# Performance work log

Hardware: AMD Instinct MI355X
Metric: run time of the kernel (lower is better)

Reference implementation:

```python
import jax, jax.numpy as jnp
import numpy as np

B, N, NUM_CLASSES = 2, 131072, 2
SCORE_THR, IOU_THR, OUT_NUM = 0.05, 0.7, 2000
NEG = -1e9  # sentinel for suppressed / below-threshold scores


def _decode(deltas, anchors):
    h = anchors[..., 2] - anchors[..., 0]
    w = anchors[..., 3] - anchors[..., 1]
    cy = (anchors[..., 2] + anchors[..., 0]) * 0.5
    cx = (anchors[..., 3] + anchors[..., 1]) * 0.5
    d = deltas * jnp.array([0.1, 0.1, 0.2, 0.2], dtype=deltas.dtype)
    cy = cy + d[..., 0] * h
    cx = cx + d[..., 1] * w
    h = h * jnp.exp(d[..., 2])
    w = w * jnp.exp(d[..., 3])
    return jnp.stack([cy - h * 0.5, cx - w * 0.5, cy + h * 0.5, cx + w * 0.5], axis=-1)


def _iou(box, boxes):
    # box [4] vs boxes [N,4] -> [N]
    y1 = jnp.maximum(box[0], boxes[:, 0])
    x1 = jnp.maximum(box[1], boxes[:, 1])
    y2 = jnp.minimum(box[2], boxes[:, 2])
    x2 = jnp.minimum(box[3], boxes[:, 3])
    inter = jnp.maximum(y2 - y1, 0.0) * jnp.maximum(x2 - x1, 0.0)
    a1 = (box[2] - box[0]) * (box[3] - box[1])
    a2 = (boxes[:, 2] - boxes[:, 0]) * (boxes[:, 3] - boxes[:, 1])
    return inter / (a1 + a2 - inter + 1e-8)


def _nms_single(boxes, scores, logits):
    # greedy NMS (= tf.image.non_max_suppression), then gather + pad_to_fixed_size
    live0 = jnp.where(scores > SCORE_THR, scores, NEG)

    def step(live, _):
        best = jnp.argmax(live)
        ok = live[best] > NEG * 0.5
        iou = _iou(boxes[best], boxes)
        live = jnp.where((iou > IOU_THR) & ok, NEG, live)
        live = live.at[best].set(NEG)
        return live, (best.astype(jnp.int32), ok.astype(boxes.dtype))

    _, (sel, valid) = jax.lax.scan(step, live0, None, length=OUT_NUM)
    vb = valid[:, None]  # [OUT_NUM,1] pad tag: 1 for real rows, 0 for padding
    out_boxes = boxes[sel] * vb
    out_scores = scores[sel][:, None] * vb
    out_logits = logits[sel] * vb
    return (jnp.concatenate([out_boxes, vb], axis=-1),
            jnp.concatenate([out_scores, vb], axis=-1),
            jnp.concatenate([out_logits, vb], axis=-1))


def _forward(deltas, class_logits, anchors):
    probs = jax.nn.softmax(class_logits, axis=-1)
    fg_scores = jnp.max(probs[..., 1:], axis=-1)  # [B,N]
    boxes = _decode(deltas, anchors)              # [B,N,4]
    return jax.vmap(_nms_single)(boxes, fg_scores, class_logits)


def setup_inputs() -> dict:
    key = jax.random.key(0)
    k1, k2, k3, k4, k5, k6 = jax.random.split(key, 6)
    deltas = jax.random.normal(k1, (B, N, 4), jnp.float32) * 0.5
    class_logits = jax.random.normal(k2, (B, N, NUM_CLASSES), jnp.float32)
    cy = jax.random.uniform(k3, (B, N), minval=0.0, maxval=800.0)
    cx = jax.random.uniform(k4, (B, N), minval=0.0, maxval=800.0)
    h = jax.random.uniform(k5, (B, N), minval=16.0, maxval=256.0)
    w = jax.random.uniform(k6, (B, N), minval=16.0, maxval=256.0)
    anchors = jnp.stack([cy - h * 0.5, cx - w * 0.5, cy + h * 0.5, cx + w * 0.5], axis=-1)
    return {"deltas": deltas, "class_logits": class_logits, "anchors": anchors}


def reference(deltas, class_logits, anchors):
    return _forward(deltas, class_logits, anchors)
```

## Files before the change

### kernel.cpp

```cpp
#include <hip/hip_runtime.h>
#include <stdint.h>
#include <stddef.h>

#define BATCH 2
#define NELEM 131072
#define OUT_NUM 2000
#define KCAP 32
#define PREWIN 16384
#define KPRE_W (PREWIN / 64)

__device__ __forceinline__ float exp32cr(float x) { return (float)exp((double)x); }

__device__ __forceinline__ bool iou_gt(float by1, float bx1, float by2, float bx2,
                                       float cy1, float cx1, float cy2, float cx2) {
    float y1 = fmaxf(by1, cy1), x1 = fmaxf(bx1, cx1);
    float y2 = fminf(by2, cy2), x2 = fminf(bx2, cx2);
    float ih = __fsub_rn(y2, y1), iw = __fsub_rn(x2, x1);
    if (ih <= 0.0f || iw <= 0.0f) return false;
    float inter = __fmul_rn(ih, iw);
    float a1 = __fmul_rn(__fsub_rn(by2, by1), __fsub_rn(bx2, bx1));
    float a2 = __fmul_rn(__fsub_rn(cy2, cy1), __fsub_rn(cx2, cx1));
    float den = __fadd_rn(__fsub_rn(__fadd_rn(a1, a2), inter), 1e-8f);
    float rhs = __fmul_rn(0.7f, den);
    if (inter > __fmul_rn(rhs, 1.0001f)) return true;
    if (inter < __fmul_rn(rhs, 0.9999f)) return false;
    return __fdiv_rn(inter, den) > 0.7f;
}
__device__ __forceinline__ bool iou_gt4(float4 a, float4 c) {
    return iou_gt(a.x, a.y, a.z, a.w, c.x, c.y, c.z, c.w);
}

__device__ __forceinline__ bool maybe4(float4 A, float4 C) {
    float dy = fabsf((A.x + A.z) - (C.x + C.z));
    float dx = fabsf((A.y + A.w) - (C.y + C.w));
    float hs = (A.z - A.x) + (C.z - C.x);
    float ws = (A.w - A.y) + (C.w - C.y);
    return (dy < 0.19f * hs) && (dx < 0.19f * ws);
}

__device__ __forceinline__ void decode_f(const float* __restrict__ deltas,
                                         const float* __restrict__ anchors,
                                         size_t gi, float* bx) {
    float a0 = anchors[4 * gi], a1 = anchors[4 * gi + 1];
    float a2 = anchors[4 * gi + 2], a3 = anchors[4 * gi + 3];
    float h = __fsub_rn(a2, a0), w = __fsub_rn(a3, a1);
    float cy = __fmul_rn(__fadd_rn(a2, a0), 0.5f);
    float cx = __fmul_rn(__fadd_rn(a3, a1), 0.5f);
    float d0 = __fmul_rn(deltas[4 * gi], 0.1f);
    float d1 = __fmul_rn(deltas[4 * gi + 1], 0.1f);
    float d2 = __fmul_rn(deltas[4 * gi + 2], 0.2f);
    float d3 = __fmul_rn(deltas[4 * gi + 3], 0.2f);
    cy = __fadd_rn(cy, __fmul_rn(d0, h));
    cx = __fadd_rn(cx, __fmul_rn(d1, w));
    h = __fmul_rn(h, exp32cr(d2));
    w = __fmul_rn(w, exp32cr(d3));
    bx[0] = __fsub_rn(cy, __fmul_rn(h, 0.5f));
    bx[1] = __fsub_rn(cx, __fmul_rn(w, 0.5f));
    bx[2] = __fadd_rn(cy, __fmul_rn(h, 0.5f));
    bx[3] = __fadd_rn(cx, __fmul_rn(w, 0.5f));
}

__device__ __forceinline__ float score_f(const float* __restrict__ logits, size_t gi) {
    float l0 = logits[2 * gi], l1 = logits[2 * gi + 1];
    float m = fmaxf(l0, l1);
    float e0 = exp32cr(__fsub_rn(l0, m));
    float e1 = exp32cr(__fsub_rn(l1, m));
    return __fdiv_rn(e1, __fadd_rn(e0, e1));
}

__global__ __launch_bounds__(256) void prep_kernel(
    const float* __restrict__ logits, uint64_t* __restrict__ keys,
    uint32_t* __restrict__ flag, uint32_t* __restrict__ state) {
    int i = blockIdx.x * 256 + threadIdx.x;
    if (i == 0) *flag = 0;
    if (i < 32) state[i] = 0;
    if (i >= BATCH * NELEM) return;
    float s = score_f(logits, (size_t)i);
    uint32_t idx = (uint32_t)(i & (NELEM - 1));
    uint64_t key = 0;
    if (s > 0.05f)
        key = ((uint64_t)__float_as_uint(s) << 17) | ((~idx) & 0x1FFFFu);
    keys[i] = key;
}

__global__ __launch_bounds__(1024) void bitonic_local_sort4(uint64_t* __restrict__ keys) {
    __shared__ uint64_t sh[4096];
    const int t = threadIdx.x;
    const size_t base = (size_t)blockIdx.x * 4096;
    for (int e = t; e < 4096; e += 1024) sh[e] = keys[base + e];
    __syncthreads();
    const int gb = (int)(base & (NELEM - 1));
    for (int k = 2; k <= 4096; k <<= 1) {
        for (int j = k >> 1; j >= 1; j >>= 1) {
            for (int pp = t; pp < 2048; pp += 1024) {
                int a = ((pp & ~(j - 1)) << 1) | (pp & (j - 1));
                bool ddd = (((gb + a) & k) == 0);
                uint64_t x = sh[a], y = sh[a + j];
                bool sw = ddd ? (x < y) : (x > y);
                if (sw) { sh[a] = y; sh[a + j] = x; }
            }
            __syncthreads();
        }
    }
    for (int e = t; e < 4096; e += 1024) keys[base + e] = sh[e];
}

__global__ __launch_bounds__(256) void bitonic_global_pass(uint64_t* __restrict__ keys,
                                                           int k, int j) {
    int tid = blockIdx.x * blockDim.x + threadIdx.x;
    const int half = NELEM / 2;
    int b = tid / half;
    int tt = tid - b * half;
    int a = ((tt & ~(j - 1)) << 1) | (tt & (j - 1));
    uint64_t* kb = keys + (size_t)b * NELEM;
    bool ddd = ((a & k) == 0);
    uint64_t x = kb[a], y = kb[a + j];
    bool sw = ddd ? (x < y) : (x > y);
    if (sw) { kb[a] = y; kb[a + j] = x; }
}

__global__ __launch_bounds__(256) void bitonic_global_fused2(uint64_t* __restrict__ keys,
                                                             int k, int j) {
    int tid = blockIdx.x * 256 + threadIdx.x;
    const int q = NELEM / 4;
    int b = tid / q;
    int tt = tid - b * q;
    int jh = j >> 1;
    int x = ((tt & ~(jh - 1)) << 2) | (tt & (jh - 1));
    uint64_t* kb = keys + (size_t)b * NELEM;
    bool ddd = ((x & k) == 0);
    uint64_t e0 = kb[x], e1 = kb[x + jh], e2 = kb[x + j], e3 = kb[x + j + jh];
    uint64_t tmp;
#define CMPEX(A, B) { bool sw = ddd ? (A < B) : (A > B); if (sw) { tmp = A; A = B; B = tmp; } }
    CMPEX(e0, e2) CMPEX(e1, e3)
    CMPEX(e0, e1) CMPEX(e2, e3)
#undef CMPEX
    kb[x] = e0; kb[x + jh] = e1; kb[x + j] = e2; kb[x + j + jh] = e3;
}

__global__ __launch_bounds__(256) void bitonic_global_fused3(uint64_t* __restrict__ keys,
                                                             int k, int j) {
    int tid = blockIdx.x * 256 + threadIdx.x;
    const int q = NELEM / 8;
    int b = tid / q;
    int tt = tid - b * q;
    int jq = j >> 2;
    int x = ((tt & ~(jq - 1)) << 3) | (tt & (jq - 1));
    uint64_t* kb = keys + (size_t)b * NELEM;
    bool ddd = ((x & k) == 0);
    uint64_t e0 = kb[x], e1 = kb[x + jq], e2 = kb[x + 2 * jq], e3 = kb[x + 3 * jq];
    uint64_t e4 = kb[x + 4 * jq], e5 = kb[x + 5 * jq], e6 = kb[x + 6 * jq], e7 = kb[x + 7 * jq];
    uint64_t tmp;
#define CMPEX(A, B) { bool sw = ddd ? (A < B) : (A > B); if (sw) { tmp = A; A = B; B = tmp; } }
    CMPEX(e0, e4) CMPEX(e1, e5) CMPEX(e2, e6) CMPEX(e3, e7)
    CMPEX(e0, e2) CMPEX(e1, e3) CMPEX(e4, e6) CMPEX(e5, e7)
    CMPEX(e0, e1) CMPEX(e2, e3) CMPEX(e4, e5) CMPEX(e6, e7)
#undef CMPEX
    kb[x] = e0; kb[x + jq] = e1; kb[x + 2 * jq] = e2; kb[x + 3 * jq] = e3;
    kb[x + 4 * jq] = e4; kb[x + 5 * jq] = e5; kb[x + 6 * jq] = e6; kb[x + 7 * jq] = e7;
}

__global__ __launch_bounds__(256) void bitonic_global_fused4(uint64_t* __restrict__ keys,
                                                             int k, int j) {
    int tid = blockIdx.x * 256 + threadIdx.x;
    const int q = NELEM / 16;
    int b = tid / q;
    int tt = tid - b * q;
    int jq = j >> 3;
    int x = ((tt & ~(jq - 1)) << 4) | (tt & (jq - 1));
    uint64_t* kb = keys + (size_t)b * NELEM;
    bool ddd = ((x & k) == 0);
    uint64_t e[16];
#pragma unroll
    for (int i = 0; i < 16; ++i) e[i] = kb[x + i * jq];
    uint64_t tmp;
#define CMPEX(A, B) { bool sw = ddd ? (e[A] < e[B]) : (e[A] > e[B]); \
    if (sw) { tmp = e[A]; e[A] = e[B]; e[B] = tmp; } }
#pragma unroll
    for (int i = 0; i < 8; ++i) CMPEX(i, i + 8)
#pragma unroll
    for (int g2 = 0; g2 < 16; g2 += 8) {
        CMPEX(g2 + 0, g2 + 4) CMPEX(g2 + 1, g2 + 5) CMPEX(g2 + 2, g2 + 6) CMPEX(g2 + 3, g2 + 7)
    }
#pragma unroll
    for (int g2 = 0; g2 < 16; g2 += 4) { CMPEX(g2 + 0, g2 + 2) CMPEX(g2 + 1, g2 + 3) }
#pragma unroll
    for (int g2 = 0; g2 < 16; g2 += 2) CMPEX(g2, g2 + 1)
#undef CMPEX
#pragma unroll
    for (int i = 0; i < 16; ++i) kb[x + i * jq] = e[i];
}

__global__ __launch_bounds__(1024) void bitonic_local_merge8(uint64_t* __restrict__ keys,
                                                             int k) {
    __shared__ uint64_t sh[8192];
    const int t = threadIdx.x;
    const size_t base = (size_t)blockIdx.x * 8192;
    for (int e = t; e < 8192; e += 1024) sh[e] = keys[base + e];
    __syncthreads();
    const bool ddd = (((int)(base & (NELEM - 1)) & k) == 0);
    for (int j = 4096; j >= 1; j >>= 1) {
        for (int pp = t; pp < 4096; pp += 1024) {
            int a = ((pp & ~(j - 1)) << 1) | (pp & (j - 1));
            uint64_t x = sh[a], y = sh[a + j];
            bool sw = ddd ? (x < y) : (x > y);
            if (sw) { sh[a] = y; sh[a + j] = x; }
        }
        __syncthreads();
    }
    for (int e = t; e < 8192; e += 1024) keys[base + e] = sh[e];
}

__global__ __launch_bounds__(256) void sort_check(const uint64_t* __restrict__ keys,
                                                  uint32_t* __restrict__ flag) {
    int i = blockIdx.x * 256 + threadIdx.x;
    if (i >= BATCH * NELEM) return;
    uint32_t q = (uint32_t)i & (NELEM - 1);
    if (q != NELEM - 1) {
        if (keys[i] < keys[i + 1]) atomicOr(flag, 1u);
    }
}

__global__ __launch_bounds__(256) void records_kernel(
    const uint64_t* __restrict__ keys, const float* __restrict__ deltas,
    const float* __restrict__ anchors, const float* __restrict__ logits,
    float* __restrict__ records, uint32_t* __restrict__ kcount, int M) {
    int g = blockIdx.x * 256 + threadIdx.x;
    if (g >= BATCH * M) return;
    kcount[g] = 0;
    int b = g / M, r = g - b * M;
    uint64_t key = keys[(size_t)b * NELEM + r];
    float4 r0, r1;
    if (key != 0) {
        uint32_t idx = (uint32_t)((~key) & 0x1FFFFu);
        size_t gi = (size_t)b * NELEM + idx;
        float bx[4];
        decode_f(deltas, anchors, gi, bx);
        r0 = make_float4(bx[0], bx[1], bx[2], bx[3]);
        r1 = make_float4(score_f(logits, gi), logits[2 * gi], logits[2 * gi + 1], 1.0f);
    } else {
        r0 = make_float4(0.f, 0.f, 0.f, 0.f);
        r1 = make_float4(0.f, 0.f, 0.f, 0.f);
    }
    float4* rp = (float4*)records;
    rp[(size_t)g * 2] = r0;
    rp[(size_t)g * 2 + 1] = r1;
}

__global__ __launch_bounds__(64) void mask_kernel(const float* __restrict__ records,
                                                  uint64_t* __restrict__ masks,
                                                  uint32_t* __restrict__ kcount,
                                                  uint16_t* __restrict__ klist, int M) {
    int ti = blockIdx.x, tj = blockIdx.y, b = blockIdx.z;
    if (tj > ti) return;
    int t = threadIdx.x;
    __shared__ float4 jb[64];
    __shared__ int jv[64];
    const float4* rp = (const float4*)records;
    {
        float4 rj  = rp[((size_t)b * M + (size_t)tj * 64 + t) * 2];
        float4 rj1 = rp[((size_t)b * M + (size_t)tj * 64 + t) * 2 + 1];
        jb[t] = rj;
        jv[t] = (rj1.w != 0.f);
    }
    const int i = ti * 64 + t;
    float4 ri  = rp[((size_t)b * M + i) * 2];
    float4 ri1 = rp[((size_t)b * M + i) * 2 + 1];
    bool iv = (ri1.w != 0.f);
    __syncthreads();
    uint64_t word = 0;
    if (iv) {
        for (int jj = 0; jj < 64; ++jj) {
            bool earlier = (tj < ti) || (jj < t);
            if (earlier && jv[jj] && maybe4(jb[jj], ri) && iou_gt4(jb[jj], ri)) {
                word |= 1ull << jj;
                uint32_t slot = atomicAdd(&kcount[(size_t)b * M + i], 1u);
                if (slot < KCAP)
                    klist[((size_t)b * M + i) * KCAP + slot] = (uint16_t)(tj * 64 + jj);
            }
        }
    }
    masks[((size_t)b * M + i) * (size_t)(M >> 6) + tj] = word;
}

__global__ void nms_walk(
    const float* __restrict__ records, const uint64_t* __restrict__ masks,
    const uint32_t* __restrict__ kcount, const uint16_t* __restrict__ klist,
    float4* __restrict__ accbox, uint32_t* __restrict__ state,
    float* __restrict__ out, int M) {
    const int b = blockIdx.x;
    const int t = threadIdx.x;
    const int Wm = M >> 6;
    const int NC = M >> 8;
    const uint64_t* mb = masks + (size_t)b * M * (size_t)Wm;
    const float4* rp = (const float4*)records + (size_t)b * M * 2;

    __shared__ uint64_t accset[128];
    __shared__ uint64_t bwLDS[256][4];
    __shared__ uint8_t kf[256];
    __shared__ float4 recLDS[512];
    __shared__ uint32_t s_state[16];

    for (int w = t; w < 128; w += blockDim.x) accset[w] = 0;
    __syncthreads();

    int n_acc = 0, done = 0;
    for (int ci = 0; ci < NC && !done; ++ci) {
        const int p = ci << 8;
        const int pw = ci << 2;
        if (t < 256) {
            const int gi = p + t;
            uint32_t cnt = kcount[(size_t)b * M + gi];
            uint64_t rq0 = 0, rq1 = 0, rq2 = 0, rq3 = 0;
            bool kill = false;
            if (cnt <= KCAP) {
                const uint16_t* lp = klist + ((size_t)b * M + gi) * KCAP;
                for (uint32_t u = 0; u < cnt; ++u) {
                    int j = lp[u];
                    if (j < p) {
                        if ((accset[j >> 6] >> (j & 63)) & 1) kill = true;
                    } else {
                        int d = j - p;
                        uint64_t bit = 1ull << (d & 63);
                        switch (d >> 6) {
                            case 0: rq0 |= bit; break;
                            case 1: rq1 |= bit; break;
                            case 2: rq2 |= bit; break;
                            default: rq3 |= bit; break;
                        }
                    }
                }
            } else {
                const uint64_t* row = mb + (size_t)gi * Wm;
                uint64_t o = 0;
                for (int w = 0; w < pw; ++w) o |= row[w] & accset[w];
                kill = (o != 0);
                rq0 = row[pw]; rq1 = row[pw + 1];
                rq2 = row[pw + 2]; rq3 = row[pw + 3];
            }
            kf[t] = kill ? 1 : 0;
            bwLDS[t][0] = rq0; bwLDS[t][1] = rq1;
            bwLDS[t][2] = rq2; bwLDS[t][3] = rq3;
        } else if (t < 512) {
            int i0 = t - 256;
            recLDS[i0] = rp[(size_t)p * 2 + i0];
            recLDS[i0 + 256] = rp[(size_t)p * 2 + i0 + 256];
        }
        __syncthreads();

        if (t < 64) {
            const int l = t;
            uint64_t b00 = bwLDS[l][0], b01 = bwLDS[l][1], b02 = bwLDS[l][2], b03 = bwLDS[l][3];
            uint64_t b10 = bwLDS[64 + l][0], b11 = bwLDS[64 + l][1], b12 = bwLDS[64 + l][2], b13 = bwLDS[64 + l][3];
            uint64_t b20 = bwLDS[128 + l][0], b21 = bwLDS[128 + l][1], b22 = bwLDS[128 + l][2], b23 = bwLDS[128 + l][3];
            uint64_t b30 = bwLDS[192 + l][0], b31 = bwLDS[192 + l][1], b32 = bwLDS[192 + l][2], b33 = bwLDS[192 + l][3];
            uint64_t vm0 = __ballot(recLDS[2 * l + 1].w != 0.f);
            uint64_t vm1 = __ballot(recLDS[2 * (64 + l) + 1].w != 0.f);
            uint64_t vm2 = __ballot(recLDS[2 * (128 + l) + 1].w != 0.f);
            uint64_t vm3 = __ballot(recLDS[2 * (192 + l) + 1].w != 0.f);
            uint64_t k0 = __ballot(kf[l] != 0);
            uint64_t k1 = __ballot(kf[64 + l] != 0);
            uint64_t k2 = __ballot(kf[128 + l] != 0);
            uint64_t k3 = __ballot(kf[192 + l] != 0);
            uint64_t e0m = __ballot((b00 | b01 | b02 | b03) == 0);
            uint64_t e1m = __ballot((b10 | b11 | b12 | b13) == 0);
            uint64_t e2m = __ballot((b20 | b21 | b22 | b23) == 0);
            uint64_t e3m = __ballot((b30 | b31 | b32 | b33) == 0);
            if (t == 0) {
                uint64_t t0 = vm0 & ~k0, t1 = vm1 & ~k1, t2 = vm2 & ~k2, t3 = vm3 & ~k3;
                uint64_t a0 = t0 & e0m, a1 = t1 & e1m, a2 = t2 & e2m, a3 = t3 & e3m;
                uint64_t c0 = t0 & ~e0m, c1 = t1 & ~e1m, c2 = t2 & ~e2m, c3 = t3 & ~e3m;
#define RESOLVE(cq, aq, base) \
    while (cq) { int cb = __builtin_ctzll(cq); cq &= cq - 1; \
        int idx = (base) + cb; \
        uint64_t w0 = bwLDS[idx][0], w1 = bwLDS[idx][1]; \
        uint64_t w2 = bwLDS[idx][2], w3 = bwLDS[idx][3]; \
        if (!((w0 & a0) | (w1 & a1) | (w2 & a2) | (w3 & a3))) aq |= (1ull << cb); }
                RESOLVE(c0, a0, 0)
                RESOLVE(c1, a1, 64)
                RESOLVE(c2, a2, 128)
                RESOLVE(c3, a3, 192)
#undef RESOLVE
                int n = n_acc;
                int dn = ((vm0 & vm1 & vm2 & vm3) != ~0ull) ? 1 : 0;
                int tot = (int)(__popcll(a0) + __popcll(a1) + __popcll(a2) + __popcll(a3));
                int rem = OUT_NUM - n;
                if (tot >= rem) {
                    int keep = rem;
#define TRUNC(w) { int pc = (int)__popcll(w); \
    if (keep >= pc) keep -= pc; \
    else { while ((int)__popcll(w) > keep) w &= ~(1ull << (63 - __builtin_clzll(w))); keep = 0; } }
                    TRUNC(a0) TRUNC(a1) TRUNC(a2) TRUNC(a3)
#undef TRUNC
                    n = OUT_NUM; dn = 1;
                } else {
                    n += tot;
                }
                s_state[0] = (uint32_t)n_acc;
                s_state[1] = (uint32_t)n;
                s_state[2] = (uint32_t)dn;
                s_state[3] = (uint32_t)a0; s_state[4] = (uint32_t)(a0 >> 32);
                s_state[5] = (uint32_t)a1; s_state[6] = (uint32_t)(a1 >> 32);
                s_state[7] = (uint32_t)a2; s_state[8] = (uint32_t)(a2 >> 32);
                s_state[9] = (uint32_t)a3; s_state[10] = (uint32_t)(a3 >> 32);
                accset[pw] = a0; accset[pw + 1] = a1;
                accset[pw + 2] = a2; accset[pw + 3] = a3;
            }
        }
        __syncthreads();
        int r0 = (int)s_state[0];
        n_acc = (int)s_state[1];
        done = (int)s_state[2];
        uint64_t amA = ((uint64_t)s_state[4] << 32) | s_state[3];
        uint64_t amB = ((uint64_t)s_state[6] << 32) | s_state[5];
        uint64_t amC = ((uint64_t)s_state[8] << 32) | s_state[7];
        uint64_t amD = ((uint64_t)s_state[10] << 32) | s_state[9];

        if (t < 256) {
            int q = t >> 6, ll = t & 63;
            uint64_t amq = q == 0 ? amA : q == 1 ? amB : q == 2 ? amC : amD;
            if ((amq >> ll) & 1) {
                int base = r0;
                if (q > 0) base += (int)__popcll(amA);
                if (q > 1) base += (int)__popcll(amB);
                if (q > 2) base += (int)__popcll(amC);
                int row = base + (int)__popcll(amq & ((1ull << ll) - 1ull));
                float4 cb = recLDS[t * 2], cm = recLDS[t * 2 + 1];
                accbox[(size_t)b * OUT_NUM + row] = cb;
                float* ob = out + ((size_t)b * OUT_NUM + row) * 5;
                ob[0] = cb.x; ob[1] = cb.y; ob[2] = cb.z; ob[3] = cb.w; ob[4] = 1.0f;
                float* os = out + (size_t)BATCH * OUT_NUM * 5 +
                            ((size_t)b * OUT_NUM + row) * 2;
                os[0] = cm.x; os[1] = 1.0f;
                float* ol = out + (size_t)BATCH * OUT_NUM * 7 +
                            ((size_t)b * OUT_NUM + row) * 3;
                ol[0] = cm.y; ol[1] = cm.z; ol[2] = 1.0f;
            }
        }
        __syncthreads();
    }
    if (t == 0) {
        state[b * 16] = (uint32_t)n_acc;
        state[b * 16 + 1] = (uint32_t)done;
    }
}

__global__ __launch_bounds__(1024) void prekill_kernel(
    const uint64_t* __restrict__ keys, const float* __restrict__ deltas,
    const float* __restrict__ anchors, const float4* __restrict__ accbox,
    const uint32_t* __restrict__ state, uint64_t* __restrict__ kpre, int Mend) {
    const int blk = blockIdx.x, b = blockIdx.y;
    const int t = threadIdx.x;
    const int c = t & 63, g = t >> 6;
    const int n1 = (int)state[b * 16];
    __shared__ float4 aF[OUT_NUM];
    __shared__ float4 jb[64];
    __shared__ uint8_t kfl[64];
    for (int r = t; r < n1; r += 1024) aF[r] = accbox[(size_t)b * OUT_NUM + r];
    if (t < 64) {
        kfl[t] = 0;
        int j = Mend + blk * 64 + t;
        uint64_t key = keys[(size_t)b * NELEM + j];
        float4 bx4 = make_float4(0.f, 0.f, 0.f, 0.f);
        if (key != 0) {
            uint32_t idx = (uint32_t)((~key) & 0x1FFFFu);
            size_t gi = (size_t)b * NELEM + idx;
            float bx[4];
            decode_f(deltas, anchors, gi, bx);
            bx4 = make_float4(bx[0], bx[1], bx[2], bx[3]);
        }
        jb[t] = bx4;
    }
    __syncthreads();
    float4 cb = jb[c];
    float csy = cb.x + cb.z, csx = cb.y + cb.w;
    float ch19 = 0.19f * (cb.z - cb.x), cw19 = 0.19f * (cb.w - cb.y);
    bool k = false;
    for (int a = g; a < n1; a += 16) {
        float4 af = aF[a];
        float asy = af.x + af.z, asx = af.y + af.w;
        float ah19 = 0.19f * (af.z - af.x), aw19 = 0.19f * (af.w - af.y);
        if (fabsf(asy - csy) < ah19 + ch19 && fabsf(asx - csx) < aw19 + cw19) {
            if (iou_gt4(af, cb)) { k = true; break; }
        }
    }
    if (k) kfl[c] = 1;
    __syncthreads();
    if (t < 64) {
        uint64_t w = __ballot(kfl[t] != 0);
        if (t == 0) kpre[(size_t)b * KPRE_W + blk] = w;
    }
}

__global__ __launch_bounds__(512) void nms_tail(
    const uint64_t* __restrict__ keys, const float* __restrict__ deltas,
    const float* __restrict__ logits, const float* __restrict__ anchors,
    const float4* __restrict__ accbox, const uint32_t* __restrict__ state,
    const uint64_t* __restrict__ kpre, float* __restrict__ out,
    int Mend, int hasPre) {
    const int b = blockIdx.x;
    const int t = threadIdx.x;
    const int l = t & 63;

    __shared__ float4 aF4[OUT_NUM];
    __shared__ float4 aS4[OUT_NUM];
    __shared__ float4 cbox[256], cmeta[256];
    __shared__ uint32_t transW[256][8];
    __shared__ uint8_t kf2[512];
    __shared__ uint64_t kpreLDS[4];
    __shared__ uint32_t s_state[16];

    if (t == 0) {
        s_state[0] = state[b * 16];
        s_state[1] = state[b * 16 + 1];
    }
    __syncthreads();
    int n_acc = (int)s_state[0];
    int done = (int)s_state[1];
    const int tailStart = n_acc;
    for (int r = t; r < n_acc; r += 512) {
        float4 ab = accbox[(size_t)b * OUT_NUM + r];
        aF4[r] = ab;
        aS4[r] = make_float4(ab.x + ab.z, ab.y + ab.w, ab.z - ab.x, ab.w - ab.y);
    }
    __syncthreads();

    for (int p = Mend; p < NELEM && !done; p += 256) {
        const bool inwin = hasPre && (p < Mend + PREWIN);
        for (int i = t; i < 2048; i += 512) ((uint32_t*)transW)[i] = 0;
        if (t < 256) {
            uint64_t key = keys[(size_t)b * NELEM + p + t];
            float4 bx4 = make_float4(0.f, 0.f, 0.f, 0.f);
            float4 mt = make_float4(0.f, 0.f, 0.f, 0.f);
            if (key != 0) {
                uint32_t idx = (uint32_t)((~key) & 0x1FFFFu);
                size_t gi = (size_t)b * NELEM + idx;
                float bx[4];
                decode_f(deltas, anchors, gi, bx);
                bx4 = make_float4(bx[0], bx[1], bx[2], bx[3]);
                mt = make_float4(score_f(logits, gi), logits[2 * gi],
                                 logits[2 * gi + 1], 1.0f);
            }
            cbox[t] = bx4; cmeta[t] = mt;
        }
        if (t < 4)
            kpreLDS[t] = inwin ? kpre[(size_t)b * KPRE_W + ((p - Mend) >> 6) + t] : 0ull;
        __syncthreads();

        {
            const int c = t & 255, g = t >> 8;
            float4 cb = cbox[c];
            bool pkc = inwin && ((kpreLDS[c >> 6] >> (c & 63)) & 1);
            bool valid = (cmeta[c].w != 0.f) && !pkc;
            float csy = cb.x + cb.z, csx = cb.y + cb.w;
            float chh = cb.z - cb.x, cww = cb.w - cb.y;
            bool k = false;
            int aStart = inwin ? tailStart : 0;
            if (valid) {
                for (int a = aStart + g; a < n_acc; a += 2) {
                    float4 as = aS4[a];
                    if (fabsf(as.x - csy) < 0.19f * (as.z + chh) &&
                        fabsf(as.y - csx) < 0.19f * (as.w + cww)) {
                        if (iou_gt4(aF4[a], cb)) { k = true; break; }
                    }
                }
            }
            kf2[t] = k ? 1 : 0;
        }
        __syncthreads();

        for (int pid = t; pid < 256 * 256; pid += 512) {
            int c0 = pid >> 8, c1 = pid & 255;
            if (c1 > c0 && cmeta[c0].w != 0.f && cmeta[c1].w != 0.f) {
                bool d0 = (inwin && ((kpreLDS[c0 >> 6] >> (c0 & 63)) & 1)) ||
                          kf2[c0] || kf2[256 + c0];
                bool d1 = (inwin && ((kpreLDS[c1 >> 6] >> (c1 & 63)) & 1)) ||
                          kf2[c1] || kf2[256 + c1];
                if (!d0 && !d1 && maybe4(cbox[c0], cbox[c1]) &&
                    iou_gt4(cbox[c0], cbox[c1]))
                    atomicOr(&transW[c1][c0 >> 5], 1u << (c0 & 31));
            }
        }
        __syncthreads();

        if (t < 64) {
            uint64_t bw00, bw01, bw02, bw03, bw10, bw11, bw12, bw13;
            uint64_t bw20, bw21, bw22, bw23, bw30, bw31, bw32, bw33;
            bw00 = ((uint64_t)transW[l][1] << 32) | transW[l][0];
            bw01 = ((uint64_t)transW[l][3] << 32) | transW[l][2];
            bw02 = ((uint64_t)transW[l][5] << 32) | transW[l][4];
            bw03 = ((uint64_t)transW[l][7] << 32) | transW[l][6];
            bw10 = ((uint64_t)transW[64 + l][1] << 32) | transW[64 + l][0];
            bw11 = ((uint64_t)transW[64 + l][3] << 32) | transW[64 + l][2];
            bw12 = ((uint64_t)transW[64 + l][5] << 32) | transW[64 + l][4];
            bw13 = ((uint64_t)transW[64 + l][7] << 32) | transW[64 + l][6];
            bw20 = ((uint64_t)transW[128 + l][1] << 32) | transW[128 + l][0];
            bw21 = ((uint64_t)transW[128 + l][3] << 32) | transW[128 + l][2];
            bw22 = ((uint64_t)transW[128 + l][5] << 32) | transW[128 + l][4];
            bw23 = ((uint64_t)transW[128 + l][7] << 32) | transW[128 + l][6];
            bw30 = ((uint64_t)transW[192 + l][1] << 32) | transW[192 + l][0];
            bw31 = ((uint64_t)transW[192 + l][3] << 32) | transW[192 + l][2];
            bw32 = ((uint64_t)transW[192 + l][5] << 32) | transW[192 + l][4];
            bw33 = ((uint64_t)transW[192 + l][7] << 32) | transW[192 + l][6];
            uint64_t vm0 = __ballot(cmeta[l].w != 0.f);
            uint64_t vm1 = __ballot(cmeta[64 + l].w != 0.f);
            uint64_t vm2 = __ballot(cmeta[128 + l].w != 0.f);
            uint64_t vm3 = __ballot(cmeta[192 + l].w != 0.f);
            uint64_t k0 = kpreLDS[0] | __ballot((kf2[l] | kf2[256 + l]) != 0);
            uint64_t k1 = kpreLDS[1] | __ballot((kf2[64 + l] | kf2[320 + l]) != 0);
            uint64_t k2 = kpreLDS[2] | __ballot((kf2[128 + l] | kf2[384 + l]) != 0);
            uint64_t k3 = kpreLDS[3] | __ballot((kf2[192 + l] | kf2[448 + l]) != 0);
            uint64_t t0 = vm0 & ~k0, t1 = vm1 & ~k1, t2 = vm2 & ~k2, t3 = vm3 & ~k3;
            uint64_t am0 = 0, am1 = 0, am2 = 0, am3 = 0;
            int n = n_acc;
            int dn = ((vm0 & vm1 & vm2 & vm3) != ~0ull);
            while (t0 | t1 | t2 | t3) {
                int qb; uint64_t w;
                if (t0)      { qb = 0; w = t0; }
                else if (t1) { qb = 1; w = t1; }
                else if (t2) { qb = 2; w = t2; }
                else         { qb = 3; w = t3; }
                int lb = __builtin_ctzll(w);
                uint64_t bit = 1ull << lb;
                if (qb == 0) { am0 |= bit; t0 &= ~bit; }
                else if (qb == 1) { am1 |= bit; t1 &= ~bit; }
                else if (qb == 2) { am2 |= bit; t2 &= ~bit; }
                else { am3 |= bit; t3 &= ~bit; }
                ++n;
                if (n == OUT_NUM) { dn = 1; break; }
                uint64_t s0 = qb == 0 ? bw00 : qb == 1 ? bw01 : qb == 2 ? bw02 : bw03;
                uint64_t s1 = qb == 0 ? bw10 : qb == 1 ? bw11 : qb == 2 ? bw12 : bw13;
                uint64_t s2 = qb == 0 ? bw20 : qb == 1 ? bw21 : qb == 2 ? bw22 : bw23;
                uint64_t s3 = qb == 0 ? bw30 : qb == 1 ? bw31 : qb == 2 ? bw32 : bw33;
                t0 &= ~__ballot(((s0 >> lb) & 1) != 0);
                t1 &= ~__ballot(((s1 >> lb) & 1) != 0);
                t2 &= ~__ballot(((s2 >> lb) & 1) != 0);
                t3 &= ~__ballot(((s3 >> lb) & 1) != 0);
            }
            if (t == 0) {
                s_state[0] = (uint32_t)n_acc;
                s_state[1] = (uint32_t)n;
                s_state[2] = (uint32_t)dn;
                s_state[3] = (uint32_t)am0; s_state[4] = (uint32_t)(am0 >> 32);
                s_state[5] = (uint32_t)am1; s_state[6] = (uint32_t)(am1 >> 32);
                s_state[7] = (uint32_t)am2; s_state[8] = (uint32_t)(am2 >> 32);
                s_state[9] = (uint32_t)am3; s_state[10] = (uint32_t)(am3 >> 32);
            }
        }
        __syncthreads();
        int r0 = (int)s_state[0];
        n_acc = (int)s_state[1];
        done = (int)s_state[2];
        uint64_t amA = ((uint64_t)s_state[4] << 32) | s_state[3];
        uint64_t amB = ((uint64_t)s_state[6] << 32) | s_state[5];
        uint64_t amC = ((uint64_t)s_state[8] << 32) | s_state[7];
        uint64_t amD = ((uint64_t)s_state[10] << 32) | s_state[9];

        if (t < 256) {
            int q = t >> 6, ll = t & 63;
            uint64_t amq = q == 0 ? amA : q == 1 ? amB : q == 2 ? amC : amD;
            if ((amq >> ll) & 1) {
                int base = r0;
                if (q > 0) base += (int)__popcll(amA);
                if (q > 1) base += (int)__popcll(amB);
                if (q > 2) base += (int)__popcll(amC);
                int row = base + (int)__popcll(amq & ((1ull << ll) - 1ull));
                float4 cb = cbox[t];
                float4 cm = cmeta[t];
                aF4[row] = cb;
                aS4[row] = make_float4(cb.x + cb.z, cb.y + cb.w,
                                       cb.z - cb.x, cb.w - cb.y);
                float* ob = out + ((size_t)b * OUT_NUM + row) * 5;
                ob[0] = cb.x; ob[1] = cb.y; ob[2] = cb.z; ob[3] = cb.w; ob[4] = 1.0f;
                float* os = out + (size_t)BATCH * OUT_NUM * 5 +
                            ((size_t)b * OUT_NUM + row) * 2;
                os[0] = cm.x; os[1] = 1.0f;
                float* ol = out + (size_t)BATCH * OUT_NUM * 7 +
                            ((size_t)b * OUT_NUM + row) * 3;
                ol[0] = cm.y; ol[1] = cm.z; ol[2] = 1.0f;
            }
        }
        __syncthreads();
    }

    for (int r = n_acc + t; r < OUT_NUM; r += 512) {
        float* ob = out + ((size_t)b * OUT_NUM + r) * 5;
        ob[0] = 0.f; ob[1] = 0.f; ob[2] = 0.f; ob[3] = 0.f; ob[4] = 0.f;
        float* os = out + (size_t)BATCH * OUT_NUM * 5 + ((size_t)b * OUT_NUM + r) * 2;
        os[0] = 0.f; os[1] = 0.f;
        float* ol = out + (size_t)BATCH * OUT_NUM * 7 + ((size_t)b * OUT_NUM + r) * 3;
        ol[0] = 0.f; ol[1] = 0.f; ol[2] = 0.f;
    }
    if (t == 0 && n_acc < OUT_NUM) out[0] = 2.0e5f;
}

__global__ void canary_kernel(const uint32_t* __restrict__ flag, float* __restrict__ out,
                              int code) {
    if (code) { out[0] = 3.0e5f; return; }
    if (*flag) out[0] = 1.0e5f;
}

extern "C" void kernel_launch(void* const* d_in, const int* in_sizes, int n_in,
                              void* d_out, int out_size, void* d_ws, size_t ws_size,
                              hipStream_t stream) {
    const float* deltas  = (const float*)d_in[0];
    const float* logits  = (const float*)d_in[1];
    const float* anchors = (const float*)d_in[2];
    float* out = (float*)d_out;

    const size_t keysB = (size_t)BATCH * NELEM * 8;
    const size_t flagOff = keysB;
    const size_t stateOff = keysB + 256;
    const size_t kpreOff = keysB + 512;
    const size_t accOff = kpreOff + 8192;
    const size_t recOff = accOff + 65536;
    if (ws_size < recOff) {
        canary_kernel<<<1, 1, 0, stream>>>((const uint32_t*)d_ws, out, 1);
        return;
    }
    int M = 0, wbs = 512;
    const int tiers[3] = {8192, 4096, 2048};
    const int twbs[3]  = {512, 576, 640};
    for (int i = 0; i < 3; ++i) {
        int cand = tiers[i];
        size_t need = recOff + (size_t)BATCH * cand * 32 +
                      (size_t)BATCH * cand * (cand / 8) +
                      (size_t)BATCH * cand * 4 +
                      (size_t)BATCH * cand * KCAP * 2;
        if (ws_size >= need) { M = cand; wbs = twbs[i]; break; }
    }

    uint64_t* keys = (uint64_t*)d_ws;
    uint32_t* flag = (uint32_t*)((char*)d_ws + flagOff);
    uint32_t* state = (uint32_t*)((char*)d_ws + stateOff);
    uint64_t* kpre = (uint64_t*)((char*)d_ws + kpreOff);
    float4* accbox = (float4*)((char*)d_ws + accOff);
    float* records = (float*)((char*)d_ws + recOff);
    uint64_t* masks = (uint64_t*)((char*)d_ws + recOff + (size_t)BATCH * M * 32);
    uint32_t* kcount = (uint32_t*)((char*)masks + (size_t)BATCH * M * (M / 8));
    uint16_t* klist = (uint16_t*)((char*)kcount + (size_t)BATCH * M * 4);

    prep_kernel<<<(BATCH * NELEM) / 256, 256, 0, stream>>>(logits, keys, flag, state);

    bitonic_local_sort4<<<BATCH * NELEM / 4096, 1024, 0, stream>>>(keys);
    bitonic_local_merge8<<<BATCH * NELEM / 8192, 1024, 0, stream>>>(keys, 8192);
    bitonic_global_pass<<<(BATCH * NELEM / 2) / 256, 256, 0, stream>>>(keys, 16384, 8192);
    bitonic_local_merge8<<<BATCH * NELEM / 8192, 1024, 0, stream>>>(keys, 16384);
    bitonic_global_fused2<<<(BATCH * NELEM / 4) / 256, 256, 0, stream>>>(keys, 32768, 16384);
    bitonic_local_merge8<<<BATCH * NELEM / 8192, 1024, 0, stream>>>(keys, 32768);
    bitonic_global_fused3<<<(BATCH * NELEM / 8) / 256, 256, 0, stream>>>(keys, 65536, 32768);
    bitonic_local_merge8<<<BATCH * NELEM / 8192, 1024, 0, stream>>>(keys, 65536);
    bitonic_global_fused4<<<(BATCH * NELEM / 16) / 256, 256, 0, stream>>>(keys, 131072, 65536);
    bitonic_local_merge8<<<BATCH * NELEM / 8192, 1024, 0, stream>>>(keys, 131072);

    sort_check<<<(BATCH * NELEM) / 256, 256, 0, stream>>>(keys, flag);
    if (M > 0) {
        records_kernel<<<(BATCH * M) / 256, 256, 0, stream>>>(keys, deltas, anchors,
                                                              logits, records, kcount, M);
        dim3 mg(M / 64, M / 64, BATCH);
        mask_kernel<<<mg, 64, 0, stream>>>(records, masks, kcount, klist, M);
        nms_walk<<<BATCH, wbs, 0, stream>>>(records, masks, kcount, klist,
                                            accbox, state, out, M);
        dim3 pg(PREWIN / 64, BATCH);
        prekill_kernel<<<pg, 1024, 0, stream>>>(keys, deltas, anchors, accbox, state,
                                                kpre, M);
    }
    nms_tail<<<BATCH, 512, 0, stream>>>(keys, deltas, logits, anchors, accbox, state,
                                        kpre, out, M, (M > 0) ? 1 : 0);
    canary_kernel<<<1, 1, 0, stream>>>(flag, out, 0);
}
```

Measured before the change: 280.6 us.

## Sort accepted boxes by y-center and binary-search candidate window in prekill

Adds a per-batch kernel that bitonic-sorts the accepted boxes by vertical center sum and records the maximum box height in the state buffer. The prekill kernel then binary-searches a y-range around each candidate box and only tests accepted boxes inside that range, instead of scanning all accepted boxes. This replaces a linear overlap scan with a bounded window. In exchange it adds one extra small launch with many shared-memory barriers. It also reorders accbox, which any later consumer of that buffer must tolerate.

```diff
diff --git a/kernel.cpp b/kernel.cpp
--- a/kernel.cpp
+++ b/kernel.cpp
@@ -445,6 +445,52 @@
     }
 }
 
+__global__ __launch_bounds__(1024) void accsort_kernel(
+    float4* __restrict__ accbox, uint32_t* __restrict__ state,
+    uint32_t* __restrict__ flag) {
+    const int b = blockIdx.x;
+    const int t = threadIdx.x;
+    const int n1 = (int)state[b * 16];
+    __shared__ uint64_t sk[2048];
+    __shared__ float4 tb[2048];
+    __shared__ uint32_t s_hmax;
+    if (t == 0) s_hmax = 0;
+    float4* base = accbox + (size_t)b * OUT_NUM;
+    for (int i = t; i < 2048; i += 1024) {
+        uint64_t key = ~0ull;
+        if (i < n1) {
+            float4 ab = base[i];
+            tb[i] = ab;
+            uint32_t sb = __float_as_uint(ab.x + ab.z);
+            sb = (sb & 0x80000000u) ? ~sb : (sb | 0x80000000u);
+            key = ((uint64_t)sb << 32) | (uint32_t)i;
+        }
+        sk[i] = key;
+    }
+    __syncthreads();
+    for (int k = 2; k <= 2048; k <<= 1) {
+        for (int j = k >> 1; j >= 1; j >>= 1) {
+            int a = ((t & ~(j - 1)) << 1) | (t & (j - 1));
+            bool up = ((a & k) == 0);
+            uint64_t x = sk[a], y = sk[a + j];
+            bool sw = up ? (x > y) : (x < y);
+            if (sw) { sk[a] = y; sk[a + j] = x; }
+            __syncthreads();
+        }
+    }
+    uint32_t hm = 0;
+    for (int i = t; i < n1; i += 1024) {
+        float4 ab = tb[(uint32_t)(sk[i] & 0xFFFFFFFFu)];
+        base[i] = ab;
+        uint32_t hb = __float_as_uint(ab.z - ab.x);
+        hm = hm > hb ? hm : hb;
+        if (i + 1 < n1 && (sk[i] >> 32) > (sk[i + 1] >> 32)) atomicOr(flag, 2u);
+    }
+    if (hm) atomicMax(&s_hmax, hm);
+    __syncthreads();
+    if (t == 0) state[b * 16 + 2] = s_hmax;
+}
+
 __global__ __launch_bounds__(1024) void prekill_kernel(
     const uint64_t* __restrict__ keys, const float* __restrict__ deltas,
     const float* __restrict__ anchors, const float4* __restrict__ accbox,
@@ -453,10 +499,16 @@
     const int t = threadIdx.x;
     const int c = t & 63, g = t >> 6;
     const int n1 = (int)state[b * 16];
+    const float ahmax = __uint_as_float(state[b * 16 + 2]);
     __shared__ float4 aF[OUT_NUM];
+    __shared__ float aSy[OUT_NUM];
     __shared__ float4 jb[64];
     __shared__ uint8_t kfl[64];
-    for (int r = t; r < n1; r += 1024) aF[r] = accbox[(size_t)b * OUT_NUM + r];
+    for (int r = t; r < n1; r += 1024) {
+        float4 ab = accbox[(size_t)b * OUT_NUM + r];
+        aF[r] = ab;
+        aSy[r] = ab.x + ab.z;
+    }
     if (t < 64) {
         kfl[t] = 0;
         int j = Mend + blk * 64 + t;
@@ -474,9 +526,18 @@
     __syncthreads();
     float4 cb = jb[c];
     float csy = cb.x + cb.z, csx = cb.y + cb.w;
-    float ch19 = 0.19f * (cb.z - cb.x), cw19 = 0.19f * (cb.w - cb.y);
+    float chh = cb.z - cb.x;
+    float ch19 = 0.19f * chh, cw19 = 0.19f * (cb.w - cb.y);
+    float R = 0.2f * (ahmax + chh);
+    float loV = csy - R, hiV = csy + R;
+    int lo = 0, hi = n1;
+    while (lo < hi) { int mid = (lo + hi) >> 1; if (aSy[mid] < loV) lo = mid + 1; else hi = mid; }
+    const int i0 = lo;
+    hi = n1;
+    while (lo < hi) { int mid = (lo + hi) >> 1; if (aSy[mid] <= hiV) lo = mid + 1; else hi = mid; }
+    const int i1 = lo;
     bool k = false;
-    for (int a = g; a < n1; a += 16) {
+    for (int a = i0 + g; a < i1; a += 16) {
         float4 af = aF[a];
         float asy = af.x + af.z, asx = af.y + af.w;
         float ah19 = 0.19f * (af.z - af.x), aw19 = 0.19f * (af.w - af.y);
@@ -761,6 +822,7 @@
         mask_kernel<<<mg, 64, 0, stream>>>(records, masks, kcount, klist, M);
         nms_walk<<<BATCH, wbs, 0, stream>>>(records, masks, kcount, klist,
                                             accbox, state, out, M);
+        accsort_kernel<<<BATCH, 1024, 0, stream>>>(accbox, state, flag);
         dim3 pg(PREWIN / 64, BATCH);
         prekill_kernel<<<pg, 1024, 0, stream>>>(keys, deltas, anchors, accbox, state,
                                                 kpre, M);
```

After: 248.6 us. -11.4%, faster.
